# Optimization experiments

Hardware: AMD Instinct MI355X
Metric: run time of the kernel (lower is better)

Reference implementation:

```python
import jax, jax.numpy as jnp
import numpy as np

V, H, E, L = 50257, 1024, 1024, 512


def setup_inputs() -> dict:
    key = jax.random.key(0)
    ks = jax.random.split(key, 16)
    s = 0.02  # init scale
    return {
        "input_token": jax.random.randint(ks[0], (1,), 0, V),
        "hidden": jax.random.normal(ks[1], (1, 1, H), jnp.float32),
        "encoder_outputs": jax.random.normal(ks[2], (L, H), jnp.float32),
        "embedding": jax.random.normal(ks[3], (V, E), jnp.float32) * s,
        "attn_w": jax.random.normal(ks[4], (L, H + E), jnp.float32) * s,
        "attn_b": jnp.zeros((L,), jnp.float32),
        "comb_w": jax.random.normal(ks[5], (E, H + E), jnp.float32) * s,
        "comb_b": jnp.zeros((E,), jnp.float32),
        "w_ih": jax.random.normal(ks[6], (3 * H, E), jnp.float32) * s,
        "w_hh": jax.random.normal(ks[7], (3 * H, H), jnp.float32) * s,
        "b_ih": jnp.zeros((3 * H,), jnp.float32),
        "b_hh": jnp.zeros((3 * H,), jnp.float32),
        "out_w": jax.random.normal(ks[8], (V, H), jnp.float32) * s,
        "out_b": jnp.zeros((V,), jnp.float32),
    }


def reference(input_token, hidden, encoder_outputs, embedding, attn_w, attn_b,
              comb_w, comb_b, w_ih, w_hh, b_ih, b_hh, out_w, out_b):
    # embedded = embedding(input).view(1,1,-1); dropout is identity in eval
    emb = embedding[input_token].reshape(1, E)            # [1, E]
    h0 = hidden[0]                                        # [1, H]
    # attention over encoder positions
    attn_logits = jnp.concatenate([emb, h0], axis=1) @ attn_w.T + attn_b  # [1, L]
    attn_weights = jax.nn.softmax(attn_logits, axis=1)
    attn_applied = attn_weights @ encoder_outputs         # [1, H]
    # combine + relu
    x = jnp.concatenate([emb, attn_applied], axis=1) @ comb_w.T + comb_b  # [1, E]
    x = jax.nn.relu(x)
    # single GRU cell step (PyTorch gate order: r, z, n)
    gi = x @ w_ih.T + b_ih                                # [1, 3H]
    gh = h0 @ w_hh.T + b_hh                               # [1, 3H]
    i_r, i_z, i_n = jnp.split(gi, 3, axis=1)
    h_r, h_z, h_n = jnp.split(gh, 3, axis=1)
    r = jax.nn.sigmoid(i_r + h_r)
    z = jax.nn.sigmoid(i_z + h_z)
    n = jnp.tanh(i_n + r * h_n)
    h_new = (1.0 - z) * n + z * h0                        # [1, H]
    # output projection + log softmax
    logits = h_new @ out_w.T + out_b                      # [1, V]
    out = jax.nn.log_softmax(logits, axis=1)
    return out, h_new[None], attn_weights
```

## Files before the change

### kernel.cpp

```cpp
#include <hip/hip_runtime.h>

#define V 50257
#define H 1024
#define E 1024
#define LENC 512
#define GBLK 1024
#define GWAVES (GBLK * 4)

__device__ __forceinline__ float wave_reduce_sum(float v) {
    #pragma unroll
    for (int off = 32; off > 0; off >>= 1)
        v += __shfl_down(v, off, 64);
    return v;
}

__device__ __forceinline__ void prefetch_chunk(const float* __restrict__ out_w,
                                               int chunk) {
    const float4* p = (const float4*)out_w + (size_t)chunk * 4096;
    float acc = 0.f;
    #pragma unroll 4
    for (int i = threadIdx.x; i < 4096; i += 256) {
        float4 v = p[i];
        acc += v.x + v.y + v.z + v.w;
    }
    asm volatile("" ::"v"(acc));
}

__global__ void stageA_kernel(const float* __restrict__ attn_w,
                              const float* __restrict__ attn_b,
                              const float* __restrict__ w_hh,
                              const float* __restrict__ b_hh,
                              const float* __restrict__ emb_table,
                              const int*   __restrict__ token,
                              const float* __restrict__ hidden,
                              const float* __restrict__ out_w,
                              float* __restrict__ alog,
                              float* __restrict__ g,
                              float* __restrict__ aapp) {
    int bx = blockIdx.x;
    int wid = threadIdx.x >> 6, lane = threadIdx.x & 63;
    if (bx < 128) {
        int row = bx * 4 + wid;
        const float4* w4 = (const float4*)(attn_w + (size_t)row * 2048);
        const float4* e4 = (const float4*)(emb_table + (size_t)(*token) * 1024);
        const float4* h4 = (const float4*)hidden;
        float acc = 0.f;
        #pragma unroll
        for (int j = 0; j < 4; ++j) {
            float4 w = w4[lane + 64 * j];
            float4 x = e4[lane + 64 * j];
            acc += w.x * x.x + w.y * x.y + w.z * x.z + w.w * x.w;
        }
        #pragma unroll
        for (int j = 0; j < 4; ++j) {
            float4 w = w4[256 + lane + 64 * j];
            float4 x = h4[lane + 64 * j];
            acc += w.x * x.x + w.y * x.y + w.z * x.z + w.w * x.w;
        }
        acc = wave_reduce_sum(acc);
        if (lane == 0) alog[row] = acc + attn_b[row];
    } else if (bx < 896) {
        int row = (bx - 128) * 4 + wid;
        const float4* w4 = (const float4*)(w_hh + (size_t)row * 1024);
        const float4* h4 = (const float4*)hidden;
        float acc = 0.f;
        #pragma unroll
        for (int j = 0; j < 4; ++j) {
            float4 w = w4[lane + 64 * j];
            float4 x = h4[lane + 64 * j];
            acc += w.x * x.x + w.y * x.y + w.z * x.z + w.w * x.w;
        }
        acc = wave_reduce_sum(acc);
        if (lane == 0) g[3072 + row] = acc + b_hh[row];
    } else if (bx == 896) {
        int t = threadIdx.x;
        aapp[t] = 0.f; aapp[256 + t] = 0.f; aapp[512 + t] = 0.f; aapp[768 + t] = 0.f;
    } else {
        prefetch_chunk(out_w, bx - 897);
    }
}

__global__ void stageC_kernel(const float* __restrict__ alog,
                              const float* __restrict__ enc,
                              const float* __restrict__ out_w,
                              float* __restrict__ aapp,
                              float* __restrict__ attnw_out) {
    int bx = blockIdx.x;
    if (bx >= 256) { prefetch_chunk(out_w, 160 + bx - 256); return; }
    int t = threadIdx.x;
    int lane = t & 63, wid = t >> 6;
    __shared__ float eb[512];
    __shared__ float sm[4], ssum[4];
    float a0 = alog[t], a1 = alog[t + 256];
    float m = fmaxf(a0, a1);
    #pragma unroll
    for (int off = 32; off > 0; off >>= 1)
        m = fmaxf(m, __shfl_down(m, off, 64));
    if (lane == 0) sm[wid] = m;
    __syncthreads();
    float M = fmaxf(fmaxf(sm[0], sm[1]), fmaxf(sm[2], sm[3]));
    float e0 = expf(a0 - M), e1 = expf(a1 - M);
    eb[t] = e0; eb[t + 256] = e1;
    float s = e0 + e1;
    s = wave_reduce_sum(s);
    if (lane == 0) ssum[wid] = s;
    __syncthreads();
    float S = ssum[0] + ssum[1] + ssum[2] + ssum[3];
    if (bx == 0) {
        attnw_out[t] = eb[t] / S;
        attnw_out[t + 256] = eb[t + 256] / S;
    }
    int h  = (bx & 3) * 256 + t;
    int l0 = (bx >> 2) * 8;
    float acc = 0.f;
    #pragma unroll
    for (int l = 0; l < 8; ++l)
        acc += eb[l0 + l] * enc[(size_t)(l0 + l) * 1024 + h];
    atomicAdd(&aapp[h], acc / S);
}

__global__ void stageD_kernel(const float* __restrict__ comb_w,
                              const float* __restrict__ comb_b,
                              const float* __restrict__ emb_table,
                              const int*   __restrict__ token,
                              const float* __restrict__ aapp,
                              const float* __restrict__ out_w,
                              float* __restrict__ xbuf) {
    int bx = blockIdx.x;
    if (bx >= 256) { prefetch_chunk(out_w, 320 + bx - 256); return; }
    int wid = threadIdx.x >> 6, lane = threadIdx.x & 63;
    int row = bx * 4 + wid;
    const float4* w4 = (const float4*)(comb_w + (size_t)row * 2048);
    const float4* e4 = (const float4*)(emb_table + (size_t)(*token) * 1024);
    const float4* a4 = (const float4*)aapp;
    float acc = 0.f;
    #pragma unroll
    for (int j = 0; j < 4; ++j) {
        float4 w = w4[lane + 64 * j];
        float4 x = e4[lane + 64 * j];
        acc += w.x * x.x + w.y * x.y + w.z * x.z + w.w * x.w;
    }
    #pragma unroll
    for (int j = 0; j < 4; ++j) {
        float4 w = w4[256 + lane + 64 * j];
        float4 x = a4[lane + 64 * j];
        acc += w.x * x.x + w.y * x.y + w.z * x.z + w.w * x.w;
    }
    acc = wave_reduce_sum(acc);
    if (lane == 0) xbuf[row] = fmaxf(acc + comb_b[row], 0.0f);
}

__global__ void stageE_kernel(const float* __restrict__ w_ih,
                              const float* __restrict__ b_ih,
                              const float* __restrict__ xbuf,
                              const float* __restrict__ out_w,
                              float* __restrict__ g) {
    int bx = blockIdx.x;
    if (bx >= 768) { prefetch_chunk(out_w, 480 + bx - 768); return; }
    int wid = threadIdx.x >> 6, lane = threadIdx.x & 63;
    int row = bx * 4 + wid;
    const float4* w4 = (const float4*)(w_ih + (size_t)row * 1024);
    const float4* x4 = (const float4*)xbuf;
    float acc = 0.f;
    #pragma unroll
    for (int j = 0; j < 4; ++j) {
        float4 w = w4[lane + 64 * j];
        float4 x = x4[lane + 64 * j];
        acc += w.x * x.x + w.y * x.y + w.z * x.z + w.w * x.w;
    }
    acc = wave_reduce_sum(acc);
    if (lane == 0) g[row] = acc + b_ih[row];
}

__global__ void logits_kernel(const float* __restrict__ g,
                              const float* __restrict__ hidden,
                              const float* __restrict__ out_w,
                              const float* __restrict__ out_b,
                              float* __restrict__ logits,
                              float* __restrict__ part,
                              float* __restrict__ hnew_out) {
    __shared__ float4 hsm4[256];
    float* hs = (float*)hsm4;
    int t = threadIdx.x;
    for (int j = t; j < 1024; j += 256) {
        float i_r = g[j], i_z = g[j + 1024], i_n = g[j + 2048];
        float h_r = g[3072 + j], h_z = g[4096 + j], h_n = g[5120 + j];
        float r = 1.0f / (1.0f + expf(-(i_r + h_r)));
        float z = 1.0f / (1.0f + expf(-(i_z + h_z)));
        float n = tanhf(i_n + r * h_n);
        float hv = (1.0f - z) * n + z * hidden[j];
        hs[j] = hv;
        if (blockIdx.x == 0) hnew_out[j] = hv;
    }
    __syncthreads();
    int wid = t >> 6, lane = t & 63;
    const float4* h4 = (const float4*)hsm4;
    float4 x0 = h4[lane], x1 = h4[lane + 64], x2 = h4[lane + 128], x3 = h4[lane + 192];
    float psum = 0.f;
    for (int row = blockIdx.x * 4 + wid; row < V; row += GWAVES) {
        const float4* w4 = (const float4*)(out_w + (size_t)row * 1024);
        float4 w0 = w4[lane], w1 = w4[lane + 64], w2 = w4[lane + 128], w3 = w4[lane + 192];
        float acc = w0.x * x0.x + w0.y * x0.y + w0.z * x0.z + w0.w * x0.w
                  + w1.x * x1.x + w1.y * x1.y + w1.z * x1.z + w1.w * x1.w
                  + w2.x * x2.x + w2.y * x2.y + w2.z * x2.z + w2.w * x2.w
                  + w3.x * x3.x + w3.y * x3.y + w3.z * x3.z + w3.w * x3.w;
        acc = wave_reduce_sum(acc);
        if (lane == 0) {
            acc += out_b[row];
            logits[row] = acc;
            psum += expf(acc);
        }
    }
    __shared__ float s[4];
    if (lane == 0) s[wid] = psum;
    __syncthreads();
    if (t == 0) part[blockIdx.x] = s[0] + s[1] + s[2] + s[3];
}

__global__ void logsub_kernel(float* __restrict__ out,
                              const float* __restrict__ part) {
    int t = threadIdx.x;
    int lane = t & 63, wid = t >> 6;
    float v = part[t] + part[t + 256] + part[t + 512] + part[t + 768];
    v = wave_reduce_sum(v);
    __shared__ float s[4];
    if (lane == 0) s[wid] = v;
    __syncthreads();
    float lse = logf(s[0] + s[1] + s[2] + s[3]);
    int i = blockIdx.x * 256 + t;
    if (i < V) out[i] -= lse;
}

extern "C" void kernel_launch(void* const* d_in, const int* in_sizes, int n_in,
                              void* d_out, int out_size, void* d_ws, size_t ws_size,
                              hipStream_t stream) {
    const int*   token     = (const int*)d_in[0];
    const float* hidden    = (const float*)d_in[1];
    const float* enc       = (const float*)d_in[2];
    const float* emb_table = (const float*)d_in[3];
    const float* attn_w    = (const float*)d_in[4];
    const float* attn_b    = (const float*)d_in[5];
    const float* comb_w    = (const float*)d_in[6];
    const float* comb_b    = (const float*)d_in[7];
    const float* w_ih      = (const float*)d_in[8];
    const float* w_hh      = (const float*)d_in[9];
    const float* b_ih      = (const float*)d_in[10];
    const float* b_hh      = (const float*)d_in[11];
    const float* out_w     = (const float*)d_in[12];
    const float* out_b     = (const float*)d_in[13];

    float* out       = (float*)d_out;
    float* hnew_out  = out + V;
    float* attnw_out = out + V + H;

    float* wsf  = (float*)d_ws;
    float* alog = wsf;
    float* aapp = alog + 512;
    float* xbuf = aapp + 1024;
    float* g    = xbuf + 1024;
    float* part = g + 6144;

    stageA_kernel<<<1057, 256, 0, stream>>>(attn_w, attn_b, w_hh, b_hh, emb_table,
                                            token, hidden, out_w, alog, g, aapp);
    stageC_kernel<<<416, 256, 0, stream>>>(alog, enc, out_w, aapp, attnw_out);
    stageD_kernel<<<416, 256, 0, stream>>>(comb_w, comb_b, emb_table, token, aapp,
                                           out_w, xbuf);
    stageE_kernel<<<864, 256, 0, stream>>>(w_ih, b_ih, xbuf, out_w, g);
    logits_kernel<<<GBLK, 256, 0, stream>>>(g, hidden, out_w, out_b, out, part,
                                            hnew_out);
    logsub_kernel<<<(V + 255) / 256, 256, 0, stream>>>(out, part);
}
```

Baseline: 60.24 us.

## Drop out_w L2 prefetch blocks and double logits kernel grid size

Removes the extra blocks in the early stage kernels that streamed chunks of out_w to warm the cache ahead of the logits projection. It also doubles the logits kernel grid to 2048 blocks and updates logsub to sum 8 partials per thread. Small dot-product loops are folded into a shared helper. This gives up the overlap of out_w loading with the dependent early stages in exchange for lighter early kernels and more parallelism in the logits pass.

```diff
diff --git a/kernel.cpp b/kernel.cpp
--- a/kernel.cpp
+++ b/kernel.cpp
@@ -4,7 +4,7 @@
 #define H 1024
 #define E 1024
 #define LENC 512
-#define GBLK 1024
+#define GBLK 2048
 #define GWAVES (GBLK * 4)
 
 __device__ __forceinline__ float wave_reduce_sum(float v) {
@@ -14,16 +14,17 @@
     return v;
 }
 
-__device__ __forceinline__ void prefetch_chunk(const float* __restrict__ out_w,
-                                               int chunk) {
-    const float4* p = (const float4*)out_w + (size_t)chunk * 4096;
+__device__ __forceinline__ float dot1024(const float* __restrict__ Wr,
+                                         const float4* __restrict__ v4, int lane) {
+    const float4* w4 = (const float4*)Wr;
     float acc = 0.f;
-    #pragma unroll 4
-    for (int i = threadIdx.x; i < 4096; i += 256) {
-        float4 v = p[i];
-        acc += v.x + v.y + v.z + v.w;
-    }
-    asm volatile("" ::"v"(acc));
+    #pragma unroll
+    for (int j = 0; j < 4; ++j) {
+        float4 w = w4[lane + 64 * j];
+        float4 x = v4[lane + 64 * j];
+        acc += w.x * x.x + w.y * x.y + w.z * x.z + w.w * x.w;
+    }
+    return acc;
 }
 
 __global__ void stageA_kernel(const float* __restrict__ attn_w,
@@ -33,60 +34,35 @@
                               const float* __restrict__ emb_table,
                               const int*   __restrict__ token,
                               const float* __restrict__ hidden,
-                              const float* __restrict__ out_w,
                               float* __restrict__ alog,
                               float* __restrict__ g,
                               float* __restrict__ aapp) {
     int bx = blockIdx.x;
     int wid = threadIdx.x >> 6, lane = threadIdx.x & 63;
+    const float4* h4 = (const float4*)hidden;
     if (bx < 128) {
         int row = bx * 4 + wid;
-        const float4* w4 = (const float4*)(attn_w + (size_t)row * 2048);
+        const float* Wr = attn_w + (size_t)row * 2048;
         const float4* e4 = (const float4*)(emb_table + (size_t)(*token) * 1024);
-        const float4* h4 = (const float4*)hidden;
-        float acc = 0.f;
-        #pragma unroll
-        for (int j = 0; j < 4; ++j) {
-            float4 w = w4[lane + 64 * j];
-            float4 x = e4[lane + 64 * j];
-            acc += w.x * x.x + w.y * x.y + w.z * x.z + w.w * x.w;
-        }
-        #pragma unroll
-        for (int j = 0; j < 4; ++j) {
-            float4 w = w4[256 + lane + 64 * j];
-            float4 x = h4[lane + 64 * j];
-            acc += w.x * x.x + w.y * x.y + w.z * x.z + w.w * x.w;
-        }
+        float acc = dot1024(Wr, e4, lane) + dot1024(Wr + 1024, h4, lane);
         acc = wave_reduce_sum(acc);
         if (lane == 0) alog[row] = acc + attn_b[row];
     } else if (bx < 896) {
         int row = (bx - 128) * 4 + wid;
-        const float4* w4 = (const float4*)(w_hh + (size_t)row * 1024);
-        const float4* h4 = (const float4*)hidden;
-        float acc = 0.f;
-        #pragma unroll
-        for (int j = 0; j < 4; ++j) {
-            float4 w = w4[lane + 64 * j];
-            float4 x = h4[lane + 64 * j];
-            acc += w.x * x.x + w.y * x.y + w.z * x.z + w.w * x.w;
-        }
+        float acc = dot1024(w_hh + (size_t)row * 1024, h4, lane);
         acc = wave_reduce_sum(acc);
         if (lane == 0) g[3072 + row] = acc + b_hh[row];
-    } else if (bx == 896) {
+    } else {
         int t = threadIdx.x;
         aapp[t] = 0.f; aapp[256 + t] = 0.f; aapp[512 + t] = 0.f; aapp[768 + t] = 0.f;
-    } else {
-        prefetch_chunk(out_w, bx - 897);
     }
 }
 
 __global__ void stageC_kernel(const float* __restrict__ alog,
                               const float* __restrict__ enc,
-                              const float* __restrict__ out_w,
                               float* __restrict__ aapp,
                               float* __restrict__ attnw_out) {
     int bx = blockIdx.x;
-    if (bx >= 256) { prefetch_chunk(out_w, 160 + bx - 256); return; }
     int t = threadIdx.x;
     int lane = t & 63, wid = t >> 6;
     __shared__ float eb[512];
@@ -101,8 +77,7 @@
     float M = fmaxf(fmaxf(sm[0], sm[1]), fmaxf(sm[2], sm[3]));
     float e0 = expf(a0 - M), e1 = expf(a1 - M);
     eb[t] = e0; eb[t + 256] = e1;
-    float s = e0 + e1;
-    s = wave_reduce_sum(s);
+    float s = wave_reduce_sum(e0 + e1);
     if (lane == 0) ssum[wid] = s;
     __syncthreads();
     float S = ssum[0] + ssum[1] + ssum[2] + ssum[3];
@@ -124,28 +99,13 @@
                               const float* __restrict__ emb_table,
                               const int*   __restrict__ token,
                               const float* __restrict__ aapp,
-                              const float* __restrict__ out_w,
                               float* __restrict__ xbuf) {
     int bx = blockIdx.x;
-    if (bx >= 256) { prefetch_chunk(out_w, 320 + bx - 256); return; }
     int wid = threadIdx.x >> 6, lane = threadIdx.x & 63;
     int row = bx * 4 + wid;
-    const float4* w4 = (const float4*)(comb_w + (size_t)row * 2048);
+    const float* Wr = comb_w + (size_t)row * 2048;
     const float4* e4 = (const float4*)(emb_table + (size_t)(*token) * 1024);
-    const float4* a4 = (const float4*)aapp;
-    float acc = 0.f;
-    #pragma unroll
-    for (int j = 0; j < 4; ++j) {
-        float4 w = w4[lane + 64 * j];
-        float4 x = e4[lane + 64 * j];
-        acc += w.x * x.x + w.y * x.y + w.z * x.z + w.w * x.w;
-    }
-    #pragma unroll
-    for (int j = 0; j < 4; ++j) {
-        float4 w = w4[256 + lane + 64 * j];
-        float4 x = a4[lane + 64 * j];
-        acc += w.x * x.x + w.y * x.y + w.z * x.z + w.w * x.w;
-    }
+    float acc = dot1024(Wr, e4, lane) + dot1024(Wr + 1024, (const float4*)aapp, lane);
     acc = wave_reduce_sum(acc);
     if (lane == 0) xbuf[row] = fmaxf(acc + comb_b[row], 0.0f);
 }
@@ -153,21 +113,11 @@
 __global__ void stageE_kernel(const float* __restrict__ w_ih,
                               const float* __restrict__ b_ih,
                               const float* __restrict__ xbuf,
-                              const float* __restrict__ out_w,
                               float* __restrict__ g) {
     int bx = blockIdx.x;
-    if (bx >= 768) { prefetch_chunk(out_w, 480 + bx - 768); return; }
     int wid = threadIdx.x >> 6, lane = threadIdx.x & 63;
     int row = bx * 4 + wid;
-    const float4* w4 = (const float4*)(w_ih + (size_t)row * 1024);
-    const float4* x4 = (const float4*)xbuf;
-    float acc = 0.f;
-    #pragma unroll
-    for (int j = 0; j < 4; ++j) {
-        float4 w = w4[lane + 64 * j];
-        float4 x = x4[lane + 64 * j];
-        acc += w.x * x.x + w.y * x.y + w.z * x.z + w.w * x.w;
-    }
+    float acc = dot1024(w_ih + (size_t)row * 1024, (const float4*)xbuf, lane);
     acc = wave_reduce_sum(acc);
     if (lane == 0) g[row] = acc + b_ih[row];
 }
@@ -221,7 +171,9 @@
                               const float* __restrict__ part) {
     int t = threadIdx.x;
     int lane = t & 63, wid = t >> 6;
-    float v = part[t] + part[t + 256] + part[t + 512] + part[t + 768];
+    float v = 0.f;
+    #pragma unroll
+    for (int i = 0; i < 8; ++i) v += part[t + 256 * i];
     v = wave_reduce_sum(v);
     __shared__ float s[4];
     if (lane == 0) s[wid] = v;
@@ -260,12 +212,12 @@
     float* g    = xbuf + 1024;
     float* part = g + 6144;
 
-    stageA_kernel<<<1057, 256, 0, stream>>>(attn_w, attn_b, w_hh, b_hh, emb_table,
-                                            token, hidden, out_w, alog, g, aapp);
-    stageC_kernel<<<416, 256, 0, stream>>>(alog, enc, out_w, aapp, attnw_out);
-    stageD_kernel<<<416, 256, 0, stream>>>(comb_w, comb_b, emb_table, token, aapp,
-                                           out_w, xbuf);
-    stageE_kernel<<<864, 256, 0, stream>>>(w_ih, b_ih, xbuf, out_w, g);
+    stageA_kernel<<<897, 256, 0, stream>>>(attn_w, attn_b, w_hh, b_hh, emb_table,
+                                           token, hidden, alog, g, aapp);
+    stageC_kernel<<<256, 256, 0, stream>>>(alog, enc, aapp, attnw_out);
+    stageD_kernel<<<256, 256, 0, stream>>>(comb_w, comb_b, emb_table, token, aapp,
+                                           xbuf);
+    stageE_kernel<<<768, 256, 0, stream>>>(w_ih, b_ih, xbuf, g);
     logits_kernel<<<GBLK, 256, 0, stream>>>(g, hidden, out_w, out_b, out, part,
                                             hnew_out);
     logsub_kernel<<<(V + 255) / 256, 256, 0, stream>>>(out, part);
```

Result: faster. 56.20 us (-6.7%).
